# Kernel optimization log

Hardware: AMD Instinct MI355X
Metric: run time of the kernel (lower is better)

The kernel has to match this reference:

```python
import jax, jax.numpy as jnp
import numpy as np

IDIM = 1024
HIDDEN = 4096
N_EXPERT = 8
T = 2048


def setup_inputs() -> dict:
    key = jax.random.key(0)
    ks = jax.random.split(key, 6)
    s_in = 1.0 / np.sqrt(IDIM)
    s_h = 1.0 / np.sqrt(HIDDEN)
    return {
        "xs": jax.random.normal(ks[0], (T, IDIM), dtype=jnp.float32),
        "top_k": 2,
        # gate: Linear(idim -> n_expert, bias=False); torch weight (E, D)
        "Wg": jax.random.uniform(ks[1], (N_EXPERT, IDIM), jnp.float32, -s_in, s_in),
        # experts stacked: w_1 Linear(idim->hidden), w_2 Linear(hidden->idim)
        "W1": jax.random.uniform(ks[2], (N_EXPERT, IDIM, HIDDEN), jnp.float32, -s_in, s_in),
        "b1": jax.random.uniform(ks[3], (N_EXPERT, HIDDEN), jnp.float32, -s_in, s_in),
        "W2": jax.random.uniform(ks[4], (N_EXPERT, HIDDEN, IDIM), jnp.float32, -s_h, s_h),
        "b2": jax.random.uniform(ks[5], (N_EXPERT, IDIM), jnp.float32, -s_h, s_h),
    }


def reference(xs, top_k, Wg, W1, b1, W2, b2):
    # Router: (T, E)
    router = xs @ Wg.T
    logits, selected = jax.lax.top_k(router, top_k)          # (T, k)
    # softmax over the top-k slot axis in fp32, cast back (matches torch)
    weights = jax.nn.softmax(logits.astype(jnp.float32), axis=-1).astype(xs.dtype)
    # combine weight per token per expert: (T, E). Tokens not routed to an
    # expert get weight 0, zeroing that expert's contribution (same math as
    # the masked gather / scatter-add in the torch loop).
    onehot = jax.nn.one_hot(selected, N_EXPERT, dtype=xs.dtype)  # (T, k, E)
    comb = jnp.einsum("tk,tke->te", weights, onehot)
    # all-expert FFN (dropout_rate = 0 -> identity)
    h = jax.nn.relu(jnp.einsum("td,edh->teh", xs, W1) + b1[None, :, :])
    y = jnp.einsum("teh,ehd->ted", h, W2) + b2[None, :, :]
    return jnp.einsum("te,ted->td", comb, y)
```

## Files before the change

### kernel.cpp

```cpp
#include <hip/hip_runtime.h>
#include <stdint.h>

#define T_TOK 2048
#define IDIM  1024
#define HID   4096
#define NE    8
#define BM    128
#define BN    128
#define BN2   64
#define BK    64
#define RMAX  5120
#define MAXTILES 40

typedef __bf16 bf16;
typedef bf16  bf16x8 __attribute__((ext_vector_type(8)));
typedef float f32x4  __attribute__((ext_vector_type(4)));

#define WS_NTILES   128
#define WS_TILE_E   192
#define WS_TILE_R   448
#define WS_TOK_E    1024
#define WS_TOK_W    17408
#define WS_ROW_TOK  33792
#define WS_ROW_W    54272
#define WS_TOK_POS  74752
#define XG_OFF      131072

__device__ __forceinline__ int xcd_remap(int orig, int nwg) {
    int q = nwg >> 3, r = nwg & 7;
    int xcd = orig & 7, idx = orig >> 3;
    return (xcd < r ? xcd * (q + 1) : r * (q + 1) + (xcd - r) * q) + idx;
}

__global__ __launch_bounds__(256) void k_router(const float* __restrict__ xs,
                                                const float* __restrict__ Wg,
                                                int* __restrict__ tok_e,
                                                float* __restrict__ tok_w) {
    __shared__ float sWg[NE * IDIM];
    for (int i = threadIdx.x; i < NE * IDIM; i += 256) sWg[i] = Wg[i];
    __syncthreads();
    int wave = threadIdx.x >> 6, lane = threadIdx.x & 63;
    int t = blockIdx.x * 4 + wave;
    if (t >= T_TOK) return;
    float p[NE];
#pragma unroll
    for (int e = 0; e < NE; e++) p[e] = 0.f;
    for (int j = 0; j < IDIM / 64; j++) {
        float x = xs[(size_t)t * IDIM + j * 64 + lane];
#pragma unroll
        for (int e = 0; e < NE; e++)
            p[e] += x * sWg[e * IDIM + j * 64 + lane];
    }
#pragma unroll
    for (int e = 0; e < NE; e++) {
        float v = p[e];
        for (int off = 32; off > 0; off >>= 1) v += __shfl_down(v, off);
        p[e] = v;
    }
    if (lane == 0) {
        int e0 = 0; float l0 = p[0];
        for (int e = 1; e < NE; e++) if (p[e] > l0) { l0 = p[e]; e0 = e; }
        int e1 = -1; float l1 = -1e30f;
        for (int e = 0; e < NE; e++) if (e != e0 && p[e] > l1) { l1 = p[e]; e1 = e; }
        if (e1 < 0) e1 = (e0 + 1) & 7;
        float z = __expf(l1 - l0);
        tok_e[2 * t]     = e0;  tok_e[2 * t + 1] = e1;
        tok_w[2 * t]     = 1.f / (1.f + z);
        tok_w[2 * t + 1] = z / (1.f + z);
    }
}

__global__ __launch_bounds__(256) void k_setup(int* __restrict__ w,
                                               float* __restrict__ wf) {
    __shared__ int cnt[NE];
    __shared__ int cur[NE];
    int tid = threadIdx.x;
    if (tid < NE) cnt[tid] = 0;
    for (int i = tid; i < RMAX; i += 256) w[WS_ROW_TOK / 4 + i] = -1;
    __syncthreads();
    for (int i = tid; i < 2 * T_TOK; i += 256)
        atomicAdd(&cnt[w[WS_TOK_E / 4 + i]], 1);
    __syncthreads();
    if (tid == 0) {
        int off = 0, nt = 0;
        for (int e = 0; e < NE; e++) {
            cur[e] = off;
            int nb = (cnt[e] + BM - 1) / BM;
            for (int b = 0; b < nb && nt < MAXTILES; b++) {
                w[WS_TILE_E / 4 + nt] = e;
                w[WS_TILE_R / 4 + nt] = off + b * BM;
                nt++;
            }
            off += nb * BM;
        }
        w[WS_NTILES / 4] = nt;
    }
    __syncthreads();
    for (int i = tid; i < 2 * T_TOK; i += 256) {
        int e   = w[WS_TOK_E / 4 + i];
        int pos = atomicAdd(&cur[e], 1);
        if (pos < RMAX) {
            w[WS_ROW_TOK / 4 + pos] = i >> 1;
            wf[WS_ROW_W / 4 + pos]  = wf[WS_TOK_W / 4 + i];
            w[WS_TOK_POS / 4 + i]   = pos;
        } else {
            w[WS_TOK_POS / 4 + i]   = 0;
        }
    }
}

__device__ inline uint4 pack8(float4 a, float4 b) {
    union { bf16 h[8]; uint4 u; } pk;
    pk.h[0] = (bf16)a.x; pk.h[1] = (bf16)a.y; pk.h[2] = (bf16)a.z; pk.h[3] = (bf16)a.w;
    pk.h[4] = (bf16)b.x; pk.h[5] = (bf16)b.y; pk.h[6] = (bf16)b.z; pk.h[7] = (bf16)b.w;
    return pk.u;
}
__device__ inline uint32_t pack2(float a, float b) {
    union { bf16 h[2]; uint32_t u; } pk;
    pk.h[0] = (bf16)a; pk.h[1] = (bf16)b;
    return pk.u;
}

__device__ __forceinline__ void g2l16(const bf16* g, bf16* l) {
    __builtin_amdgcn_global_load_lds(
        (const __attribute__((address_space(1))) void*)g,
        (__attribute__((address_space(3))) void*)l, 16, 0, 0);
}

__global__ __launch_bounds__(256) void k_gather(const float* __restrict__ xs,
                                                const int* __restrict__ wsi,
                                                bf16* __restrict__ Xg) {
    int wv = threadIdx.x >> 6, lane = threadIdx.x & 63;
    int r = blockIdx.x * 4 + wv;
    int tok = wsi[WS_ROW_TOK / 4 + r];
#pragma unroll
    for (int i = 0; i < 2; i++) {
        int c = i * 64 + lane;
        uint4 v;
        if (tok >= 0) {
            const float* g = xs + (size_t)tok * IDIM + c * 8;
            v = pack8(*(const float4*)g, *(const float4*)(g + 4));
        } else v = make_uint4(0u, 0u, 0u, 0u);
        int cs = (c & ~7) | ((c & 7) ^ (r & 7));
        *(uint4*)&Xg[(size_t)r * IDIM + cs * 8] = v;
    }
}

__global__ __launch_bounds__(256) void k_cvt(const float* __restrict__ src,
                                             bf16* __restrict__ dst,
                                             int ld_src, int k0, int n0, int KL,
                                             size_t s_estride, size_t d_estride,
                                             int tpb) {
    __shared__ bf16 sT[64 * 66];
    int e = blockIdx.z;
    const float* S = src + (size_t)e * s_estride;
    bf16* D = dst + (size_t)e * d_estride;
    int tn  = blockIdx.x;
    int tk0 = blockIdx.y * tpb;
    int t = threadIdx.x;
    for (int tt = 0; tt < tpb; tt++) {
        int tk = tk0 + tt;
        if (tt) __syncthreads();
#pragma unroll
        for (int i = 0; i < 4; i++) {
            int idx = t + i * 256;
            int k = idx >> 4, n4 = (idx & 15) * 4;
            float4 v = *(const float4*)&S[(size_t)(k0 + tk * 64 + k) * ld_src +
                                          n0 + tn * 64 + n4];
            *(uint32_t*)&sT[k * 66 + n4]     = pack2(v.x, v.y);
            *(uint32_t*)&sT[k * 66 + n4 + 2] = pack2(v.z, v.w);
        }
        __syncthreads();
#pragma unroll
        for (int j = 0; j < 2; j++) {
            int idx = t + j * 256;
            int n = idx >> 3, kq = idx & 7;
            union { bf16 h[8]; uint4 u; } pk;
#pragma unroll
            for (int jj = 0; jj < 8; jj++) pk.h[jj] = sT[(kq * 8 + jj) * 66 + n];
            int ng = tn * 64 + n;
            int ch = kq ^ (ng & 7);
            *(uint4*)&D[(size_t)ng * KL + tk * 64 + ch * 8] = pk.u;
        }
    }
}

__global__ __launch_bounds__(256) void k_ffn1n(const bf16* __restrict__ Xg,
                                               const bf16* __restrict__ W1t,
                                               const float* __restrict__ b1,
                                               const int* __restrict__ wsi,
                                               bf16* __restrict__ H,
                                               int h0, int CW) {
    int gx = gridDim.x;
    int orig = blockIdx.x + gx * blockIdx.y;
    int wgid = xcd_remap(orig, gx * gridDim.y);
    int bx = wgid % gx, tile = wgid / gx;
    if (tile >= wsi[WS_NTILES / 4]) return;
    int e    = wsi[WS_TILE_E / 4 + tile];
    int row0 = wsi[WS_TILE_R / 4 + tile];
    int n0   = bx * BN;

    const bf16* Abase = Xg + (size_t)row0 * IDIM;
    const bf16* Bbase = W1t + ((size_t)e * CW + n0) * IDIM;

    __shared__ bf16 smem[BM * BK + BN * BK];
    bf16* sA = smem;
    bf16* sB = smem + BM * BK;

    int t = threadIdx.x, lane = t & 63;
    int wv = t >> 6, wx = wv & 1, wy = wv >> 1;
    int lm = lane & 15, q = lane >> 4;

    f32x4 acc[4][4];
#pragma unroll
    for (int i = 0; i < 4; i++)
#pragma unroll
        for (int j = 0; j < 4; j++) acc[i][j] = (f32x4){0.f, 0.f, 0.f, 0.f};

    for (int kc = 0; kc < IDIM / BK; kc++) {
        if (kc) __syncthreads();
#pragma unroll
        for (int i = 0; i < 4; i++) {
            int s = t + i * 256;
            g2l16(Abase + (size_t)(s >> 3) * IDIM + kc * BK + (s & 7) * 8,
                  &sA[s * 8]);
        }
#pragma unroll
        for (int i = 0; i < 4; i++) {
            int s = t + i * 256;
            g2l16(Bbase + (size_t)(s >> 3) * IDIM + kc * BK + (s & 7) * 8,
                  &sB[s * 8]);
        }
        __syncthreads();
#pragma unroll
        for (int ks = 0; ks < 2; ks++) {
            bf16x8 aF[4], bF[4];
#pragma unroll
            for (int mt = 0; mt < 4; mt++) {
                int r = wy * 64 + mt * 16 + lm;
                aF[mt] = *(const bf16x8*)&sA[r * BK + (((ks * 4 + q) ^ (r & 7)) * 8)];
            }
#pragma unroll
            for (int nt = 0; nt < 4; nt++) {
                int r = wx * 64 + nt * 16 + lm;
                bF[nt] = *(const bf16x8*)&sB[r * BK + (((ks * 4 + q) ^ (r & 7)) * 8)];
            }
#pragma unroll
            for (int mt = 0; mt < 4; mt++)
#pragma unroll
                for (int nt = 0; nt < 4; nt++)
                    acc[mt][nt] = __builtin_amdgcn_mfma_f32_16x16x32_bf16(
                        aF[mt], bF[nt], acc[mt][nt], 0, 0, 0);
        }
    }

    __syncthreads();
    bf16* sC = smem;
#pragma unroll
    for (int nt = 0; nt < 4; nt++) {
        int col_l = wx * 64 + nt * 16 + lm;
        float bv  = b1[(size_t)e * HID + h0 + n0 + col_l];
#pragma unroll
        for (int mt = 0; mt < 4; mt++) {
#pragma unroll
            for (int r = 0; r < 4; r++) {
                int rloc = wy * 64 + mt * 16 + q * 4 + r;
                int rg   = row0 + rloc;
                float v = fmaxf(acc[mt][nt][r] + bv, 0.f);
                int sc = (col_l & ~63) | ((col_l & 63) ^ ((rg & 7) << 3));
                sC[rloc * BN + sc] = (bf16)v;
            }
        }
    }
    __syncthreads();
#pragma unroll
    for (int i = 0; i < 8; i++) {
        int u = t + i * 256;
        int row = u >> 4, c = u & 15;
        uint4 v = *(const uint4*)&sC[row * BN + c * 8];
        *(uint4*)&H[(size_t)(row0 + row) * CW + n0 + c * 8] = v;
    }
}

__global__ __launch_bounds__(256) void k_ffn2y(const bf16* __restrict__ H,
                                               const bf16* __restrict__ W2t,
                                               const float* __restrict__ b2,
                                               const int* __restrict__ wsi,
                                               float* __restrict__ Y,
                                               int CW, int first) {
    int gx = gridDim.x;
    int orig = blockIdx.x + gx * blockIdx.y;
    int wgid = xcd_remap(orig, gx * gridDim.y);
    int bx = wgid % gx, tile = wgid / gx;
    if (tile >= wsi[WS_NTILES / 4]) return;
    int e    = wsi[WS_TILE_E / 4 + tile];
    int row0 = wsi[WS_TILE_R / 4 + tile];
    int n0   = bx * BN2;

    const bf16* Abase = H + (size_t)row0 * CW;
    const bf16* Bbase = W2t + ((size_t)e * IDIM + n0) * CW;

    __shared__ bf16 sA[BM * BK];
    __shared__ bf16 sB[BN2 * BK];

    int t = threadIdx.x, lane = t & 63;
    int wv = t >> 6, wx = wv & 1, wy = wv >> 1;
    int lm = lane & 15, q = lane >> 4;

    f32x4 acc[4][2];
#pragma unroll
    for (int i = 0; i < 4; i++)
#pragma unroll
        for (int j = 0; j < 2; j++) acc[i][j] = (f32x4){0.f, 0.f, 0.f, 0.f};

    int kiters = CW / BK;
    for (int kc = 0; kc < kiters; kc++) {
        if (kc) __syncthreads();
#pragma unroll
        for (int i = 0; i < 4; i++) {
            int s = t + i * 256;
            g2l16(Abase + (size_t)(s >> 3) * CW + kc * BK + (s & 7) * 8,
                  &sA[s * 8]);
        }
#pragma unroll
        for (int i = 0; i < 2; i++) {
            int s = t + i * 256;
            g2l16(Bbase + (size_t)(s >> 3) * CW + kc * BK + (s & 7) * 8,
                  &sB[s * 8]);
        }
        __syncthreads();
#pragma unroll
        for (int ks = 0; ks < 2; ks++) {
            bf16x8 aF[4], bF[2];
#pragma unroll
            for (int mt = 0; mt < 4; mt++) {
                int r = wy * 64 + mt * 16 + lm;
                aF[mt] = *(const bf16x8*)&sA[r * BK + (((ks * 4 + q) ^ (r & 7)) * 8)];
            }
#pragma unroll
            for (int nt = 0; nt < 2; nt++) {
                int r = wx * 32 + nt * 16 + lm;
                bF[nt] = *(const bf16x8*)&sB[r * BK + (((ks * 4 + q) ^ (r & 7)) * 8)];
            }
#pragma unroll
            for (int mt = 0; mt < 4; mt++)
#pragma unroll
                for (int nt = 0; nt < 2; nt++)
                    acc[mt][nt] = __builtin_amdgcn_mfma_f32_16x16x32_bf16(
                        aF[mt], bF[nt], acc[mt][nt], 0, 0, 0);
        }
    }

#pragma unroll
    for (int nt = 0; nt < 2; nt++) {
        int col  = n0 + wx * 32 + nt * 16 + lm;
        float bv = first ? b2[(size_t)e * IDIM + col] : 0.f;
#pragma unroll
        for (int mt = 0; mt < 4; mt++)
#pragma unroll
            for (int r = 0; r < 4; r++) {
                int rg = row0 + wy * 64 + mt * 16 + q * 4 + r;
                float* p = &Y[(size_t)rg * IDIM + col];
                float v  = acc[mt][nt][r] + bv;
                *p = first ? v : (*p + v);
            }
    }
}

__global__ __launch_bounds__(256) void k_combine(const float* __restrict__ Y,
                                                 const int* __restrict__ wsi,
                                                 const float* __restrict__ wsf,
                                                 float* __restrict__ out) {
    int tok = blockIdx.x;
    int p0 = wsi[WS_TOK_POS / 4 + 2 * tok];
    int p1 = wsi[WS_TOK_POS / 4 + 2 * tok + 1];
    float w0 = wsf[WS_TOK_W / 4 + 2 * tok];
    float w1 = wsf[WS_TOK_W / 4 + 2 * tok + 1];
    int c = threadIdx.x;
    const float4* y0 = (const float4*)(Y + (size_t)p0 * IDIM);
    const float4* y1 = (const float4*)(Y + (size_t)p1 * IDIM);
    float4 a = y0[c], b = y1[c];
    float4 r;
    r.x = w0 * a.x + w1 * b.x;
    r.y = w0 * a.y + w1 * b.y;
    r.z = w0 * a.z + w1 * b.z;
    r.w = w0 * a.w + w1 * b.w;
    ((float4*)(out + (size_t)tok * IDIM))[c] = r;
}

__global__ __launch_bounds__(256) void k_fallback(const float* __restrict__ xs,
                                                  const float* __restrict__ Wg,
                                                  const float* __restrict__ W1,
                                                  const float* __restrict__ b1,
                                                  const float* __restrict__ W2,
                                                  const float* __restrict__ b2,
                                                  float* __restrict__ out) {
    __shared__ float xbuf[IDIM];
    __shared__ float hbuf[256];
    __shared__ float slog[NE];
    __shared__ int   sel[2];
    __shared__ float selw[2];

    int t   = blockIdx.x;
    int tid = threadIdx.x;

    for (int i = tid; i < IDIM; i += 256)
        xbuf[i] = xs[(size_t)t * IDIM + i];
    __syncthreads();
    {
        int e = tid >> 5, l = tid & 31;
        float p = 0.f;
        for (int d = l; d < IDIM; d += 32)
            p += xbuf[d] * Wg[e * IDIM + d];
        for (int off = 16; off > 0; off >>= 1) p += __shfl_down(p, off, 32);
        if (l == 0) slog[e] = p;
    }
    __syncthreads();
    if (tid == 0) {
        int e0 = 0; float l0 = slog[0];
        for (int e = 1; e < NE; e++) if (slog[e] > l0) { l0 = slog[e]; e0 = e; }
        int e1 = -1; float l1 = -1e30f;
        for (int e = 0; e < NE; e++) if (e != e0 && slog[e] > l1) { l1 = slog[e]; e1 = e; }
        if (e1 < 0) e1 = (e0 + 1) & 7;
        float z = __expf(l1 - l0);
        sel[0] = e0; sel[1] = e1;
        selw[0] = 1.f / (1.f + z);
        selw[1] = z / (1.f + z);
    }
    __syncthreads();

    float ytot[4] = {0.f, 0.f, 0.f, 0.f};
#pragma unroll
    for (int s = 0; s < 2; s++) {
        int   e = sel[s];
        float w = selw[s];
        const float* W1e = W1 + (size_t)e * IDIM * HID;
        const float* W2e = W2 + (size_t)e * HID * IDIM;
        float ys[4] = {0.f, 0.f, 0.f, 0.f};
        for (int hb = 0; hb < HID / 256; hb++) {
            int h = hb * 256 + tid;
            float acc = b1[e * HID + h];
            for (int d = 0; d < IDIM; d++)
                acc += xbuf[d] * W1e[(size_t)d * HID + h];
            __syncthreads();
            hbuf[tid] = fmaxf(acc, 0.f);
            __syncthreads();
            for (int hh = 0; hh < 256; hh++) {
                float hv = hbuf[hh];
                const float* wrow = W2e + (size_t)(hb * 256 + hh) * IDIM;
#pragma unroll
                for (int cc = 0; cc < 4; cc++)
                    ys[cc] += hv * wrow[cc * 256 + tid];
            }
        }
#pragma unroll
        for (int cc = 0; cc < 4; cc++)
            ytot[cc] += w * (ys[cc] + b2[e * IDIM + cc * 256 + tid]);
    }
#pragma unroll
    for (int cc = 0; cc < 4; cc++)
        out[(size_t)t * IDIM + cc * 256 + tid] = ytot[cc];
}

extern "C" void kernel_launch(void* const* d_in, const int* in_sizes, int n_in,
                              void* d_out, int out_size, void* d_ws, size_t ws_size,
                              hipStream_t stream) {
    int o = (n_in >= 7 && in_sizes[1] == 1) ? 1 : 0;
    const float* xs = (const float*)d_in[0];
    const float* Wg = (const float*)d_in[1 + o];
    const float* W1 = (const float*)d_in[2 + o];
    const float* b1 = (const float*)d_in[3 + o];
    const float* W2 = (const float*)d_in[4 + o];
    const float* b2 = (const float*)d_in[5 + o];
    float* out = (float*)d_out;

    size_t xg_sz = (size_t)RMAX * IDIM * 2;
    size_t y_sz  = (size_t)RMAX * IDIM * 4;
    int CW = 0;
    if (d_ws) {
        for (int c = HID; c >= 512; c >>= 1) {
            size_t need = (size_t)XG_OFF + xg_sz + (size_t)RMAX * c * 2 +
                          (size_t)NE * c * IDIM * 2 + y_sz;
            if (ws_size >= need) { CW = c; break; }
        }
    }
    if (!CW) {
        k_fallback<<<T_TOK, 256, 0, stream>>>(xs, Wg, W1, b1, W2, b2, out);
        return;
    }

    char*  ws  = (char*)d_ws;
    int*   wsi = (int*)d_ws;
    float* wsf = (float*)d_ws;
    bf16*  Xg  = (bf16*)(ws + XG_OFF);
    bf16*  Hb  = (bf16*)(ws + XG_OFF + xg_sz);
    bf16*  Wt  = (bf16*)(ws + XG_OFF + xg_sz + (size_t)RMAX * CW * 2);
    float* Yb  = (float*)(ws + XG_OFF + xg_sz + (size_t)RMAX * CW * 2 +
                          (size_t)NE * CW * IDIM * 2);

    k_router<<<T_TOK / 4, 256, 0, stream>>>(xs, Wg, wsi + WS_TOK_E / 4,
                                            wsf + WS_TOK_W / 4);
    k_setup<<<1, 256, 0, stream>>>(wsi, wsf);
    k_gather<<<RMAX / 4, 256, 0, stream>>>(xs, wsi, Xg);

    int HC = HID / CW;
    for (int c = 0; c < HC; c++) {
        {
            int ntn = CW / 64, ntk = IDIM / 64;
            int tpb = ntk;
            while (ntn * NE * (ntk / tpb) < 1024 && tpb > 1) tpb >>= 1;
            k_cvt<<<dim3(ntn, ntk / tpb, NE), 256, 0, stream>>>(
                W1, Wt, HID, 0, c * CW, IDIM,
                (size_t)IDIM * HID, (size_t)CW * IDIM, tpb);
        }
        k_ffn1n<<<dim3(CW / BN, MAXTILES), 256, 0, stream>>>(
            Xg, Wt, b1, wsi, Hb, c * CW, CW);
        {
            int ntn = IDIM / 64, ntk = CW / 64;
            int tpb = ntk;
            while (ntn * NE * (ntk / tpb) < 1024 && tpb > 1) tpb >>= 1;
            k_cvt<<<dim3(ntn, ntk / tpb, NE), 256, 0, stream>>>(
                W2, Wt, IDIM, c * CW, 0, CW,
                (size_t)HID * IDIM, (size_t)IDIM * CW, tpb);
        }
        k_ffn2y<<<dim3(IDIM / BN2, MAXTILES), 256, 0, stream>>>(
            Hb, Wt, b2, wsi, Yb, CW, c == 0 ? 1 : 0);
    }
    k_combine<<<T_TOK, 256, 0, stream>>>(Yb, wsi, wsf, out);
}
```

Baseline: 438.2 us.

## Fuse fp32-to-bf16 weight conversion into FFN GEMM kernels

Drops the separate transpose/convert kernels for W1 and W2 and instead loads fp32 weight tiles directly into LDS, converting to bf16 while building MFMA fragments. This removes a full pass writing and re-reading bf16 weight copies and the workspace they need. In exchange, each GEMM tile loads twice the bytes for B, uses more LDS, and does strided scalar LDS reads plus conversions in the inner loop.

Result: slower. 451.9 us (+3.1%).

```diff
diff --git a/kernel.cpp b/kernel.cpp
--- a/kernel.cpp
+++ b/kernel.cpp
@@ -115,16 +115,24 @@
     pk.h[4] = (bf16)b.x; pk.h[5] = (bf16)b.y; pk.h[6] = (bf16)b.z; pk.h[7] = (bf16)b.w;
     return pk.u;
 }
-__device__ inline uint32_t pack2(float a, float b) {
-    union { bf16 h[2]; uint32_t u; } pk;
-    pk.h[0] = (bf16)a; pk.h[1] = (bf16)b;
-    return pk.u;
-}
 
 __device__ __forceinline__ void g2l16(const bf16* g, bf16* l) {
     __builtin_amdgcn_global_load_lds(
         (const __attribute__((address_space(1))) void*)g,
         (__attribute__((address_space(3))) void*)l, 16, 0, 0);
+}
+__device__ __forceinline__ void g2l16f(const float* g, float* l) {
+    __builtin_amdgcn_global_load_lds(
+        (const __attribute__((address_space(1))) void*)g,
+        (__attribute__((address_space(3))) void*)l, 16, 0, 0);
+}
+
+__device__ __forceinline__ bf16x8 ldB8(const float* sBf, int n, int kbase,
+                                       int ldn) {
+    bf16x8 r;
+#pragma unroll
+    for (int j = 0; j < 8; j++) r[j] = (bf16)sBf[(kbase + j) * ldn + n];
+    return r;
 }
 
 __global__ __launch_bounds__(256) void k_gather(const float* __restrict__ xs,
@@ -146,47 +154,8 @@
     }
 }
 
-__global__ __launch_bounds__(256) void k_cvt(const float* __restrict__ src,
-                                             bf16* __restrict__ dst,
-                                             int ld_src, int k0, int n0, int KL,
-                                             size_t s_estride, size_t d_estride,
-                                             int tpb) {
-    __shared__ bf16 sT[64 * 66];
-    int e = blockIdx.z;
-    const float* S = src + (size_t)e * s_estride;
-    bf16* D = dst + (size_t)e * d_estride;
-    int tn  = blockIdx.x;
-    int tk0 = blockIdx.y * tpb;
-    int t = threadIdx.x;
-    for (int tt = 0; tt < tpb; tt++) {
-        int tk = tk0 + tt;
-        if (tt) __syncthreads();
-#pragma unroll
-        for (int i = 0; i < 4; i++) {
-            int idx = t + i * 256;
-            int k = idx >> 4, n4 = (idx & 15) * 4;
-            float4 v = *(const float4*)&S[(size_t)(k0 + tk * 64 + k) * ld_src +
-                                          n0 + tn * 64 + n4];
-            *(uint32_t*)&sT[k * 66 + n4]     = pack2(v.x, v.y);
-            *(uint32_t*)&sT[k * 66 + n4 + 2] = pack2(v.z, v.w);
-        }
-        __syncthreads();
-#pragma unroll
-        for (int j = 0; j < 2; j++) {
-            int idx = t + j * 256;
-            int n = idx >> 3, kq = idx & 7;
-            union { bf16 h[8]; uint4 u; } pk;
-#pragma unroll
-            for (int jj = 0; jj < 8; jj++) pk.h[jj] = sT[(kq * 8 + jj) * 66 + n];
-            int ng = tn * 64 + n;
-            int ch = kq ^ (ng & 7);
-            *(uint4*)&D[(size_t)ng * KL + tk * 64 + ch * 8] = pk.u;
-        }
-    }
-}
-
 __global__ __launch_bounds__(256) void k_ffn1n(const bf16* __restrict__ Xg,
-                                               const bf16* __restrict__ W1t,
+                                               const float* __restrict__ W1,
                                                const float* __restrict__ b1,
                                                const int* __restrict__ wsi,
                                                bf16* __restrict__ H,
@@ -200,12 +169,11 @@
     int row0 = wsi[WS_TILE_R / 4 + tile];
     int n0   = bx * BN;
 
-    const bf16* Abase = Xg + (size_t)row0 * IDIM;
-    const bf16* Bbase = W1t + ((size_t)e * CW + n0) * IDIM;
-
-    __shared__ bf16 smem[BM * BK + BN * BK];
-    bf16* sA = smem;
-    bf16* sB = smem + BM * BK;
+    const bf16*  Abase = Xg + (size_t)row0 * IDIM;
+    const float* Bbase = W1 + (size_t)e * IDIM * HID + h0 + n0;
+
+    __shared__ bf16  sA[BM * BK];
+    __shared__ float sBf[BK * BN];
 
     int t = threadIdx.x, lane = t & 63;
     int wv = t >> 6, wx = wv & 1, wy = wv >> 1;
@@ -226,10 +194,10 @@
                   &sA[s * 8]);
         }
 #pragma unroll
-        for (int i = 0; i < 4; i++) {
-            int s = t + i * 256;
-            g2l16(Bbase + (size_t)(s >> 3) * IDIM + kc * BK + (s & 7) * 8,
-                  &sB[s * 8]);
+        for (int i = 0; i < 8; i++) {
+            int u = t + i * 256;
+            g2l16f(Bbase + (size_t)(kc * BK + (u >> 5)) * HID + (u & 31) * 4,
+                   &sBf[u * 4]);
         }
         __syncthreads();
 #pragma unroll
@@ -241,10 +209,8 @@
                 aF[mt] = *(const bf16x8*)&sA[r * BK + (((ks * 4 + q) ^ (r & 7)) * 8)];
             }
 #pragma unroll
-            for (int nt = 0; nt < 4; nt++) {
-                int r = wx * 64 + nt * 16 + lm;
-                bF[nt] = *(const bf16x8*)&sB[r * BK + (((ks * 4 + q) ^ (r & 7)) * 8)];
-            }
+            for (int nt = 0; nt < 4; nt++)
+                bF[nt] = ldB8(sBf, wx * 64 + nt * 16 + lm, ks * 32 + q * 8, BN);
 #pragma unroll
             for (int mt = 0; mt < 4; mt++)
 #pragma unroll
@@ -255,7 +221,7 @@
     }
 
     __syncthreads();
-    bf16* sC = smem;
+    bf16* sC = (bf16*)sBf;
 #pragma unroll
     for (int nt = 0; nt < 4; nt++) {
         int col_l = wx * 64 + nt * 16 + lm;
@@ -283,11 +249,11 @@
 }
 
 __global__ __launch_bounds__(256) void k_ffn2y(const bf16* __restrict__ H,
-                                               const bf16* __restrict__ W2t,
+                                               const float* __restrict__ W2,
                                                const float* __restrict__ b2,
                                                const int* __restrict__ wsi,
                                                float* __restrict__ Y,
-                                               int CW, int first) {
+                                               int h0, int CW, int first) {
     int gx = gridDim.x;
     int orig = blockIdx.x + gx * blockIdx.y;
     int wgid = xcd_remap(orig, gx * gridDim.y);
@@ -297,11 +263,11 @@
     int row0 = wsi[WS_TILE_R / 4 + tile];
     int n0   = bx * BN2;
 
-    const bf16* Abase = H + (size_t)row0 * CW;
-    const bf16* Bbase = W2t + ((size_t)e * IDIM + n0) * CW;
-
-    __shared__ bf16 sA[BM * BK];
-    __shared__ bf16 sB[BN2 * BK];
+    const bf16*  Abase = H + (size_t)row0 * CW;
+    const float* Bbase = W2 + (size_t)e * HID * IDIM + (size_t)h0 * IDIM + n0;
+
+    __shared__ bf16  sA[BM * BK];
+    __shared__ float sBf[BK * BN2];
 
     int t = threadIdx.x, lane = t & 63;
     int wv = t >> 6, wx = wv & 1, wy = wv >> 1;
@@ -323,10 +289,10 @@
                   &sA[s * 8]);
         }
 #pragma unroll
-        for (int i = 0; i < 2; i++) {
-            int s = t + i * 256;
-            g2l16(Bbase + (size_t)(s >> 3) * CW + kc * BK + (s & 7) * 8,
-                  &sB[s * 8]);
+        for (int i = 0; i < 4; i++) {
+            int u = t + i * 256;
+            g2l16f(Bbase + (size_t)(kc * BK + (u >> 4)) * IDIM + (u & 15) * 4,
+                   &sBf[u * 4]);
         }
         __syncthreads();
 #pragma unroll
@@ -338,10 +304,8 @@
                 aF[mt] = *(const bf16x8*)&sA[r * BK + (((ks * 4 + q) ^ (r & 7)) * 8)];
             }
 #pragma unroll
-            for (int nt = 0; nt < 2; nt++) {
-                int r = wx * 32 + nt * 16 + lm;
-                bF[nt] = *(const bf16x8*)&sB[r * BK + (((ks * 4 + q) ^ (r & 7)) * 8)];
-            }
+            for (int nt = 0; nt < 2; nt++)
+                bF[nt] = ldB8(sBf, wx * 32 + nt * 16 + lm, ks * 32 + q * 8, BN2);
 #pragma unroll
             for (int mt = 0; mt < 4; mt++)
 #pragma unroll
@@ -479,8 +443,7 @@
     int CW = 0;
     if (d_ws) {
         for (int c = HID; c >= 512; c >>= 1) {
-            size_t need = (size_t)XG_OFF + xg_sz + (size_t)RMAX * c * 2 +
-                          (size_t)NE * c * IDIM * 2 + y_sz;
+            size_t need = (size_t)XG_OFF + xg_sz + (size_t)RMAX * c * 2 + y_sz;
             if (ws_size >= need) { CW = c; break; }
         }
     }
@@ -494,9 +457,7 @@
     float* wsf = (float*)d_ws;
     bf16*  Xg  = (bf16*)(ws + XG_OFF);
     bf16*  Hb  = (bf16*)(ws + XG_OFF + xg_sz);
-    bf16*  Wt  = (bf16*)(ws + XG_OFF + xg_sz + (size_t)RMAX * CW * 2);
-    float* Yb  = (float*)(ws + XG_OFF + xg_sz + (size_t)RMAX * CW * 2 +
-                          (size_t)NE * CW * IDIM * 2);
+    float* Yb  = (float*)(ws + XG_OFF + xg_sz + (size_t)RMAX * CW * 2);
 
     k_router<<<T_TOK / 4, 256, 0, stream>>>(xs, Wg, wsi + WS_TOK_E / 4,
                                             wsf + WS_TOK_W / 4);
@@ -505,26 +466,10 @@
 
     int HC = HID / CW;
     for (int c = 0; c < HC; c++) {
-        {
-            int ntn = CW / 64, ntk = IDIM / 64;
-            int tpb = ntk;
-            while (ntn * NE * (ntk / tpb) < 1024 && tpb > 1) tpb >>= 1;
-            k_cvt<<<dim3(ntn, ntk / tpb, NE), 256, 0, stream>>>(
-                W1, Wt, HID, 0, c * CW, IDIM,
-                (size_t)IDIM * HID, (size_t)CW * IDIM, tpb);
-        }
         k_ffn1n<<<dim3(CW / BN, MAXTILES), 256, 0, stream>>>(
-            Xg, Wt, b1, wsi, Hb, c * CW, CW);
-        {
-            int ntn = IDIM / 64, ntk = CW / 64;
-            int tpb = ntk;
-            while (ntn * NE * (ntk / tpb) < 1024 && tpb > 1) tpb >>= 1;
-            k_cvt<<<dim3(ntn, ntk / tpb, NE), 256, 0, stream>>>(
-                W2, Wt, IDIM, c * CW, 0, CW,
-                (size_t)HID * IDIM, (size_t)IDIM * CW, tpb);
-        }
+            Xg, W1, b1, wsi, Hb, c * CW, CW);
         k_ffn2y<<<dim3(IDIM / BN2, MAXTILES), 256, 0, stream>>>(
-            Hb, Wt, b2, wsi, Yb, CW, c == 0 ? 1 : 0);
+            Hb, W2, b2, wsi, Yb, c * CW, CW, c == 0 ? 1 : 0);
     }
     k_combine<<<T_TOK, 256, 0, stream>>>(Yb, wsi, wsf, out);
 }
```
